# Performance work log

Hardware: AMD Instinct MI355X
Metric: run time of the kernel (lower is better)

## Reference

```python
import jax, jax.numpy as jnp
import numpy as np

B, F_C, F_F = 2, 32768, 131072
C_IN, C_OUT, W_DIM, COLOR = 128, 64, 512, 3
K2 = 9
PAD0, PAD1 = 192, 384
ACT_GAIN = float(np.sqrt(2.0))  # lrelu def_gain


def _gather(x, nbr, is_pad, pad):
    # x: [N, C]; nbr: [M, k] indices into [N + pad]; is_pad: [M, k] bool
    padded = jnp.concatenate([x, jnp.zeros((pad, x.shape[1]), x.dtype)], 0)
    g = padded[nbr]  # [M, k, C]
    return jnp.where(is_pad[..., None], jnp.zeros((), x.dtype), g)


def _affine(w, aw, ab):
    # StyleGAN FullyConnectedLayer: runtime weight gain 1/sqrt(fan_in), bias_init=1
    return w @ (aw.T * (1.0 / np.sqrt(aw.shape[1]))) + ab


def _modconv(xg, weight, styles, demodulate=True):
    # xg: [N, k, I]; weight: [O, I, 1, k]; styles: [B, I]
    n, k, ci = xg.shape
    w = weight[:, :, 0, :][None, :, :, :] * styles[:, None, :, None]  # [B,O,I,k]
    if demodulate:
        w = w * jax.lax.rsqrt(jnp.sum(w * w, axis=(2, 3), keepdims=True) + 1e-8)
    xb = xg.reshape(styles.shape[0], -1, k, ci)  # [B,F,k,I]
    return jnp.einsum('bfki,boik->bfo', xb, w).reshape(n, -1)


def _smooth_upsample(x, nbr, is_pad, pad, pool_map):
    # upsample coarse->fine via parent map, then masked neighborhood mean
    xf = x[pool_map]  # [N_fine, C]
    g = _gather(xf, nbr, is_pad, pad)  # [N_fine, k, C]
    cnt = jnp.maximum(jnp.sum(~is_pad, axis=1), 1).astype(x.dtype)
    return jnp.sum(g, axis=1) / cnt[:, None]


def _act(x, gain):
    # clamp_gain(lrelu(x), act_gain*gain, 256*gain)
    y = jnp.where(x >= 0, x, 0.2 * x)
    return jnp.clip(y * (ACT_GAIN * gain), -256.0 * gain, 256.0 * gain)


def setup_inputs():
    key = jax.random.key(0)
    ks = jax.random.split(key, 16)
    x = jax.random.normal(ks[0], (B * F_C, C_IN), jnp.float32)
    img = jax.random.normal(ks[1], (B * F_C, COLOR), jnp.float32)
    ws = jax.random.normal(ks[2], (B, 3, W_DIM), jnp.float32)
    fn0 = jax.random.randint(ks[3], (B * F_C, K2), 0, B * F_C + PAD0, jnp.int32)
    fn1 = jax.random.randint(ks[4], (B * F_F, K2), 0, B * F_F + PAD1, jnp.int32)
    fip0 = jax.random.bernoulli(ks[5], 0.05, (B * F_C, K2))
    fip1 = jax.random.bernoulli(ks[6], 0.05, (B * F_F, K2))
    pool_map0 = jax.random.randint(ks[7], (B * F_F,), 0, B * F_C, jnp.int32)
    a0_w = jax.random.normal(ks[8], (C_IN, W_DIM), jnp.float32)
    a0_b = jnp.ones((C_IN,), jnp.float32)
    W0 = jax.random.normal(ks[9], (C_OUT, C_IN, 1, K2), jnp.float32)
    b0 = jnp.zeros((C_OUT,), jnp.float32)
    ns0 = jnp.zeros((1,), jnp.float32)
    nc0 = jax.random.normal(ks[10], (F_F,), jnp.float32)
    a1_w = jax.random.normal(ks[11], (C_OUT, W_DIM), jnp.float32)
    a1_b = jnp.ones((C_OUT,), jnp.float32)
    W1 = jax.random.normal(ks[12], (C_OUT, C_OUT, 1, K2), jnp.float32)
    b1 = jnp.zeros((C_OUT,), jnp.float32)
    ns1 = jnp.zeros((1,), jnp.float32)
    nc1 = jax.random.normal(ks[13], (F_F,), jnp.float32)
    at_w = jax.random.normal(ks[14], (C_OUT, W_DIM), jnp.float32)
    at_b = jnp.ones((C_OUT,), jnp.float32)
    Wt = jax.random.normal(ks[15], (COLOR, C_OUT, 1, 1), jnp.float32)
    bt = jnp.zeros((COLOR,), jnp.float32)
    return {"x": x, "img": img, "ws": ws, "a0_w": a0_w, "a0_b": a0_b, "W0": W0,
            "b0": b0, "ns0": ns0, "nc0": nc0, "a1_w": a1_w, "a1_b": a1_b,
            "W1": W1, "b1": b1, "ns1": ns1, "nc1": nc1, "at_w": at_w,
            "at_b": at_b, "Wt": Wt, "bt": bt, "fn0": fn0, "fip0": fip0,
            "fn1": fn1, "fip1": fip1, "pool_map0": pool_map0,
            "pad0": PAD0, "pad1": PAD1}


def reference(x, img, ws, a0_w, a0_b, W0, b0, ns0, nc0, a1_w, a1_b, W1, b1, ns1,
              nc1, at_w, at_b, Wt, bt, fn0, fip0, fn1, fip1, pool_map0, pad0, pad1):
    b = ws.shape[0]
    w0, w1, w2 = ws[:, 0], ws[:, 1], ws[:, 2]
    # conv0: coarse gather -> mod conv -> smooth upsample to fine -> noise/bias/act
    s0 = _affine(w0, a0_w, a0_b)
    noise0 = jnp.tile(nc0[None, :], (b, 1)).reshape(-1, 1) * ns0  # noise_mode='const'
    h = _modconv(_gather(x, fn0, fip0, pad0), W0, s0)
    h = _smooth_upsample(h, fn1, fip1, pad1, pool_map0)
    h = _act(h + noise0 + b0[None, :], 1.0)
    # conv1: fine level, no resampler
    s1 = _affine(w1, a1_w, a1_b)
    noise1 = jnp.tile(nc1[None, :], (b, 1)).reshape(-1, 1) * ns1
    h = _modconv(_gather(h, fn1, fip1, pad1), W1, s1)
    h = _act(h + noise1 + b1[None, :], 1.0)
    # torgb: kernel_size=1 -> self index only, no demodulation
    st = _affine(w2, at_w, at_b) * (1.0 / np.sqrt(C_OUT))
    y = _modconv(_gather(h, fn1[:, :1], fip1[:, :1], pad1), Wt, st, demodulate=False)
    y = jnp.clip(y + bt[None, :], -256.0, 256.0)
    img = _smooth_upsample(img, fn1, fip1, pad1, pool_map0) + y
    return (h, img)
```

## Files before the change

### kernel.cpp

```cpp
#include <hip/hip_runtime.h>
#include <hip/hip_bf16.h>

constexpr int F_C   = 32768;
constexpr int F_F   = 131072;
constexpr int N0    = 65536;
constexpr int N1    = 262144;
constexpr int C_IN  = 128;
constexpr int W_DIM = 512;
constexpr int K2c   = 9;
constexpr float RS512     = 0.04419417382415922f;
constexpr float ACT_GAINc = 1.4142135623730951f;

constexpr size_t FO_S0  = 0;
constexpr size_t FO_S1  = 256;
constexpr size_t FO_ST  = 384;
constexpr size_t OFF_WM0T = 2048;
constexpr size_t OFF_WM1T = OFF_WM0T + 294912;
constexpr size_t OFF_H0   = 458752;
constexpr size_t OFF_HA   = OFF_H0 + (size_t)8388608;
constexpr size_t OFF_YPRE = OFF_H0;
constexpr size_t OFF_XB   = OFF_HA;

typedef short s16x8 __attribute__((ext_vector_type(8)));
typedef float f32x4 __attribute__((ext_vector_type(4)));

__device__ __forceinline__ float b2f(unsigned short u) {
    union { unsigned int i; float f; } v; v.i = ((unsigned int)u) << 16; return v.f;
}
__device__ __forceinline__ unsigned short f2b(float f) {
    __hip_bfloat16 h = __float2bfloat16(f);
    return *reinterpret_cast<unsigned short*>(&h);
}
__device__ __forceinline__ float waveRedSum(float v) {
    for (int m = 32; m; m >>= 1) v += __shfl_xor(v, m, 64);
    return v;
}
__device__ __forceinline__ float actf(float v) {
    float y = (v >= 0.f) ? v : 0.2f * v;
    y *= ACT_GAINc;
    return fminf(fmaxf(y, -256.f), 256.f);
}

__global__ __launch_bounds__(64)
void k_styles(const float* __restrict__ wsF,
              const float* __restrict__ a0w, const float* __restrict__ a0b,
              const float* __restrict__ a1w, const float* __restrict__ a1b,
              const float* __restrict__ atw, const float* __restrict__ atb,
              float* __restrict__ fr)
{
    int bid = blockIdx.x, lane = threadIdx.x;
    int bb, ii, ll, row; const float *aw, *ab; float* dst; float post = 1.f;
    if (bid < 256)      { bb = bid >> 7;             ii = bid & 127; ll = 0; aw = a0w; ab = a0b; dst = fr + FO_S0; row = 128; }
    else if (bid < 384) { int t = bid - 256; bb = t >> 6; ii = t & 63; ll = 1; aw = a1w; ab = a1b; dst = fr + FO_S1; row = 64; }
    else                { int t = bid - 384; bb = t >> 6; ii = t & 63; ll = 2; aw = atw; ab = atb; dst = fr + FO_ST; row = 64; post = 0.125f; }
    const float* wsv = wsF + (size_t)(bb * 3 + ll) * W_DIM;
    const float* awr = aw + (size_t)ii * W_DIM;
    float s = 0.f;
    for (int j = lane; j < W_DIM; j += 64) s += wsv[j] * awr[j];
    s = waveRedSum(s);
    if (lane == 0) dst[bb * row + ii] = (s * RS512 + ab[ii]) * post;
}

__global__ __launch_bounds__(256)
void k_wmod(const float* __restrict__ W0,
            const float* __restrict__ W1,
            const float* __restrict__ fr,
            unsigned short* __restrict__ wm0T,
            unsigned short* __restrict__ wm1T)
{
    int bo = blockIdx.x, tid = threadIdx.x;
    int b, o, CI, NE; const float* W; const float* S; unsigned short* dst;
    if (bo < 128) { b = bo >> 6; o = bo & 63; CI = 128; NE = 1152; W = W0; S = fr + FO_S0; dst = wm0T; }
    else { int t = bo - 128; b = t >> 6; o = t & 63; CI = 64; NE = 576; W = W1; S = fr + FO_S1; dst = wm1T; }
    const float* Wo = W + (size_t)o * NE;
    const float* Sb = S + (size_t)b * CI;
    float ss = 0.f;
    for (int idx = tid; idx < NE; idx += 256) {
        int i = idx / K2c;
        float p = Wo[idx] * Sb[i];
        ss += p * p;
    }
    __shared__ float red[4];
    float s = waveRedSum(ss);
    if ((tid & 63) == 0) red[tid >> 6] = s;
    __syncthreads();
    float d = rsqrtf(red[0] + red[1] + red[2] + red[3] + 1e-8f);
    for (int idx = tid; idx < NE; idx += 256) {
        int i = idx / K2c, kk = idx - i * K2c;
        dst[((size_t)(b * K2c + kk) * 64 + o) * CI + i] = f2b(Wo[idx] * Sb[i] * d);
    }
}

__global__ __launch_bounds__(256)
void k_xcvt(const float* __restrict__ xF, unsigned short* __restrict__ xB)
{
    int i = blockIdx.x * 256 + threadIdx.x;
    float4 f = ((const float4*)xF)[i];
    union { unsigned short u[4]; uint2 v; } t;
    t.u[0] = f2b(f.x); t.u[1] = f2b(f.y); t.u[2] = f2b(f.z); t.u[3] = f2b(f.w);
    ((uint2*)xB)[i] = t.v;
}

__global__ __launch_bounds__(256, 4)
void k_layer0(const unsigned short* __restrict__ xB,
              const int*  __restrict__ fn0,
              const int*  __restrict__ fip0,
              const unsigned short* __restrict__ wm0T,
              unsigned short* __restrict__ h0B)
{
    __shared__ unsigned short W_lds[9 * 64 * 64];
    const int tid  = threadIdx.x;
    const int g0   = blockIdx.x * 256;
    const int b    = g0 / F_C;
    const int wave = tid >> 6, lane = tid & 63;
    const int lg   = lane >> 4, lr = lane & 15;
    const int wbase = g0 + wave * 64;
    const unsigned short* wtap = wm0T + (size_t)b * K2c * 64 * C_IN;

    int nbrk[4][9];
    #pragma unroll
    for (int rg = 0; rg < 4; ++rg) {
        int row = wbase + rg * 16 + lr;
        #pragma unroll
        for (int k = 0; k < 9; ++k) {
            int fn = fn0[(size_t)row * 9 + k];
            int ip = fip0[(size_t)row * 9 + k];
            nbrk[rg][k] = (!ip && fn < N0) ? fn : -1;
        }
    }

    f32x4 acc[4][4] = {};
    for (int h = 0; h < 2; ++h) {
        __syncthreads();
        #pragma unroll
        for (int t = 0; t < 18; ++t) {
            int idx = tid + 256 * t;
            int tap = idx >> 9;
            int rem = idx & 511;
            int row = rem >> 3, cc = rem & 7;
            uint4 v = *(const uint4*)(wtap + ((size_t)tap * 64 + row) * C_IN + h * 64 + cc * 8);
            *(uint4*)(&W_lds[tap * 4096 + row * 64 + ((cc ^ (row & 7)) << 3)]) = v;
        }
        __syncthreads();
        #pragma unroll
        for (int kk = 0; kk < 9; ++kk) {
            s16x8 bf[2][4];
            #pragma unroll
            for (int c2 = 0; c2 < 2; ++c2)
                #pragma unroll
                for (int nt = 0; nt < 4; ++nt) {
                    int row = nt * 16 + lr;
                    bf[c2][nt] = *(const s16x8*)(&W_lds[kk * 4096 + row * 64 + (((c2 * 4 + lg) ^ (row & 7)) << 3)]);
                }
            #pragma unroll
            for (int rg = 0; rg < 4; ++rg) {
                int nbr = nbrk[rg][kk];
                int pc  = nbr >= 0 ? nbr : 0;
                const uint4* ap = (const uint4*)(xB + (size_t)pc * C_IN) + lg;
                uint4 a0 = ap[h * 8];
                uint4 a1 = ap[h * 8 + 4];
                if (nbr < 0) { a0 = uint4{0,0,0,0}; a1 = uint4{0,0,0,0}; }
                s16x8 af0 = *reinterpret_cast<const s16x8*>(&a0);
                s16x8 af1 = *reinterpret_cast<const s16x8*>(&a1);
                #pragma unroll
                for (int nt = 0; nt < 4; ++nt)
                    acc[rg][nt] = __builtin_amdgcn_mfma_f32_16x16x32_bf16(af0, bf[0][nt], acc[rg][nt], 0, 0, 0);
                #pragma unroll
                for (int nt = 0; nt < 4; ++nt)
                    acc[rg][nt] = __builtin_amdgcn_mfma_f32_16x16x32_bf16(af1, bf[1][nt], acc[rg][nt], 0, 0, 0);
            }
        }
    }
    #pragma unroll
    for (int rg = 0; rg < 4; ++rg)
        #pragma unroll
        for (int nt = 0; nt < 4; ++nt) {
            int o = nt * 16 + lr;
            #pragma unroll
            for (int r = 0; r < 4; ++r) {
                int node = wbase + rg * 16 + lg * 4 + r;
                h0B[(size_t)node * 64 + o] = f2b(acc[rg][nt][r]);
            }
        }
}

__global__ __launch_bounds__(256)
void k_ha(const unsigned short* __restrict__ h0B,
          const int*  __restrict__ fn1,
          const int*  __restrict__ fip1,
          const int*  __restrict__ pool,
          const float* __restrict__ nc0,
          const float* __restrict__ ns0,
          const float* __restrict__ b0,
          unsigned short* __restrict__ haB)
{
    __shared__ int   pmArr[288];
    __shared__ int   vArr[288];
    __shared__ float invCnt[32];
    const int tid = threadIdx.x;
    const int n0  = blockIdx.x * 32;
    for (int idx = tid; idx < 288; idx += 256) {
        int fn = fn1[(size_t)n0 * K2c + idx];
        int ip = fip1[(size_t)n0 * K2c + idx];
        int v  = !ip;
        int pm = -1;
        if (v && fn < N1) pm = pool[fn];
        pmArr[idx] = pm;
        vArr[idx]  = v;
    }
    __syncthreads();
    if (tid < 32) {
        int c = 0;
        #pragma unroll
        for (int k = 0; k < K2c; ++k) c += vArr[tid * K2c + k];
        invCnt[tid] = 1.f / (float)(c > 0 ? c : 1);
    }
    __syncthreads();
    const int wave = tid >> 6, lane = tid & 63;
    const float nsc  = ns0[0];
    const float bias = b0[lane];
    for (int jj = 0; jj < 8; ++jj) {
        int node = wave * 8 + jj;
        int g    = n0 + node;
        float acc = 0.f;
        #pragma unroll
        for (int k = 0; k < K2c; ++k) {
            int pm = pmArr[node * K2c + k];
            int pc = pm >= 0 ? pm : 0;
            float val = b2f(h0B[(size_t)pc * 64 + lane]);
            acc += (pm >= 0) ? val : 0.f;
        }
        float hu = acc * invCnt[node];
        float v  = hu + nc0[g & (F_F - 1)] * nsc + bias;
        haB[(size_t)g * 64 + lane] = f2b(actf(v));
    }
}

__global__ __launch_bounds__(512, 4)
void k_layer1(const unsigned short* __restrict__ haB,
              const int*  __restrict__ fn1,
              const int*  __restrict__ fip1,
              const unsigned short* __restrict__ wm1T,
              const float* __restrict__ nc1,
              const float* __restrict__ ns1,
              const float* __restrict__ b1,
              const float* __restrict__ stS,
              const float* __restrict__ WtF,
              float* __restrict__ hOut,
              float* __restrict__ yPre2)
{
    __shared__ unsigned short W_lds[9 * 64 * 64];
    const int tid  = threadIdx.x;
    const int g0   = blockIdx.x * 512;
    const int b    = g0 / F_F;
    const int wave = tid >> 6, lane = tid & 63;
    const int lg   = lane >> 4, lr = lane & 15;
    const int wbase = g0 + wave * 64;
    const unsigned short* wtap = wm1T + (size_t)b * K2c * 4096;

    #pragma unroll
    for (int t = 0; t < 9; ++t) {
        int idx = tid + 512 * t;
        int tap = idx >> 9;
        int rem = idx & 511;
        int row = rem >> 3, c = rem & 7;
        uint4 v = ((const uint4*)wtap)[idx];
        *(uint4*)(&W_lds[tap * 4096 + row * 64 + ((c ^ (row & 7)) << 3)]) = v;
    }

    int nbrk[4][9];
    #pragma unroll
    for (int rg = 0; rg < 4; ++rg) {
        int row = wbase + rg * 16 + lr;
        #pragma unroll
        for (int k = 0; k < 9; ++k) {
            int fn = fn1[(size_t)row * 9 + k];
            int ip = fip1[(size_t)row * 9 + k];
            nbrk[rg][k] = (!ip && fn < N1) ? fn : -1;
        }
    }
    __syncthreads();

    f32x4 acc[4][4] = {};
    #pragma unroll
    for (int kk = 0; kk < 9; ++kk) {
        s16x8 bf[2][4];
        #pragma unroll
        for (int h = 0; h < 2; ++h)
            #pragma unroll
            for (int nt = 0; nt < 4; ++nt) {
                int row = nt * 16 + lr;
                bf[h][nt] = *(const s16x8*)(&W_lds[kk * 4096 + row * 64 + (((h * 4 + lg) ^ (row & 7)) << 3)]);
            }
        #pragma unroll
        for (int rg = 0; rg < 4; ++rg) {
            int nbr = nbrk[rg][kk];
            int pc  = nbr >= 0 ? nbr : 0;
            const uint4* ap = (const uint4*)(haB + (size_t)pc * 64) + lg;
            uint4 a0 = ap[0], a1 = ap[4];
            if (nbr < 0) { a0 = uint4{0,0,0,0}; a1 = uint4{0,0,0,0}; }
            s16x8 af0 = *reinterpret_cast<const s16x8*>(&a0);
            s16x8 af1 = *reinterpret_cast<const s16x8*>(&a1);
            #pragma unroll
            for (int nt = 0; nt < 4; ++nt)
                acc[rg][nt] = __builtin_amdgcn_mfma_f32_16x16x32_bf16(af0, bf[0][nt], acc[rg][nt], 0, 0, 0);
            #pragma unroll
            for (int nt = 0; nt < 4; ++nt)
                acc[rg][nt] = __builtin_amdgcn_mfma_f32_16x16x32_bf16(af1, bf[1][nt], acc[rg][nt], 0, 0, 0);
        }
    }

    const float nsc = ns1[0];
    #pragma unroll
    for (int rg = 0; rg < 4; ++rg) {
        float p00[4] = {}, p01[4] = {}, p02[4] = {};
        float p10[4] = {}, p11[4] = {}, p12[4] = {};
        #pragma unroll
        for (int nt = 0; nt < 4; ++nt) {
            int o = nt * 16 + lr;
            float bias = b1[o];
            float st0  = stS[o], st1 = stS[64 + o];
            float wt0 = WtF[o], wt1 = WtF[64 + o], wt2 = WtF[128 + o];
            float w00 = wt0 * st0, w01 = wt1 * st0, w02 = wt2 * st0;
            float w10 = wt0 * st1, w11 = wt1 * st1, w12 = wt2 * st1;
            #pragma unroll
            for (int r = 0; r < 4; ++r) {
                int node = wbase + rg * 16 + lg * 4 + r;
                float v  = actf(acc[rg][nt][r] + nc1[node & (F_F - 1)] * nsc + bias);
                hOut[(size_t)node * 64 + o] = v;
                p00[r] += v * w00; p01[r] += v * w01; p02[r] += v * w02;
                p10[r] += v * w10; p11[r] += v * w11; p12[r] += v * w12;
            }
        }
        #pragma unroll
        for (int m = 1; m < 16; m <<= 1) {
            #pragma unroll
            for (int r = 0; r < 4; ++r) {
                p00[r] += __shfl_xor(p00[r], m, 64);
                p01[r] += __shfl_xor(p01[r], m, 64);
                p02[r] += __shfl_xor(p02[r], m, 64);
                p10[r] += __shfl_xor(p10[r], m, 64);
                p11[r] += __shfl_xor(p11[r], m, 64);
                p12[r] += __shfl_xor(p12[r], m, 64);
            }
        }
        if (lr == 0) {
            #pragma unroll
            for (int r = 0; r < 4; ++r) {
                int node = wbase + rg * 16 + lg * 4 + r;
                yPre2[(size_t)node * 6 + 0] = p00[r];
                yPre2[(size_t)node * 6 + 1] = p01[r];
                yPre2[(size_t)node * 6 + 2] = p02[r];
                yPre2[(size_t)node * 6 + 3] = p10[r];
                yPre2[(size_t)node * 6 + 4] = p11[r];
                yPre2[(size_t)node * 6 + 5] = p12[r];
            }
        }
    }
}

__global__ __launch_bounds__(256)
void k_rgb(const float* __restrict__ yPre2,
           const float* __restrict__ imgF,
           const int*  __restrict__ fn1,
           const int*  __restrict__ fip1,
           const int*  __restrict__ pool,
           const float* __restrict__ btF,
           float* __restrict__ outImg)
{
    const int n = blockIdx.x * 256 + threadIdx.x;
    const int bOut = n / F_F;
    int fn[K2c], ip[K2c];
    #pragma unroll
    for (int k = 0; k < K2c; ++k) {
        fn[k] = fn1[(size_t)n * K2c + k];
        ip[k] = fip1[(size_t)n * K2c + k];
    }
    int pm[K2c], cnt = 0;
    #pragma unroll
    for (int k = 0; k < K2c; ++k) {
        int v  = !ip[k];
        cnt   += v;
        pm[k]  = (v && fn[k] < N1) ? pool[fn[k]] : -1;
    }
    float sr = 0.f, sg = 0.f, sb = 0.f;
    #pragma unroll
    for (int k = 0; k < K2c; ++k) {
        int   pc = pm[k] >= 0 ? pm[k] : 0;
        float m  = pm[k] >= 0 ? 1.f : 0.f;
        sr += m * imgF[(size_t)pc * 3 + 0];
        sg += m * imgF[(size_t)pc * 3 + 1];
        sb += m * imgF[(size_t)pc * 3 + 2];
    }
    int nb0 = (!ip[0] && fn[0] < N1) ? fn[0] : -1;
    float y0 = 0.f, y1 = 0.f, y2 = 0.f;
    if (nb0 >= 0) {
        const float* yp = yPre2 + (size_t)nb0 * 6 + bOut * 3;
        y0 = yp[0]; y1 = yp[1]; y2 = yp[2];
    }
    float ic = 1.f / (float)(cnt > 0 ? cnt : 1);
    y0 = fminf(fmaxf(y0 + btF[0], -256.f), 256.f);
    y1 = fminf(fmaxf(y1 + btF[1], -256.f), 256.f);
    y2 = fminf(fmaxf(y2 + btF[2], -256.f), 256.f);
    outImg[(size_t)n * 3 + 0] = sr * ic + y0;
    outImg[(size_t)n * 3 + 1] = sg * ic + y1;
    outImg[(size_t)n * 3 + 2] = sb * ic + y2;
}

extern "C" void kernel_launch(void* const* d_in, const int* in_sizes, int n_in,
                              void* d_out, int out_size, void* d_ws, size_t ws_size,
                              hipStream_t stream)
{
    const float* xF   = (const float*)d_in[0];
    const float* imgF = (const float*)d_in[1];
    const float* wsF  = (const float*)d_in[2];
    const float* a0w  = (const float*)d_in[3];
    const float* a0b  = (const float*)d_in[4];
    const float* W0w  = (const float*)d_in[5];
    const float* b0w  = (const float*)d_in[6];
    const float* ns0  = (const float*)d_in[7];
    const float* nc0  = (const float*)d_in[8];
    const float* a1w  = (const float*)d_in[9];
    const float* a1b  = (const float*)d_in[10];
    const float* W1w  = (const float*)d_in[11];
    const float* b1w  = (const float*)d_in[12];
    const float* ns1  = (const float*)d_in[13];
    const float* nc1  = (const float*)d_in[14];
    const float* atw  = (const float*)d_in[15];
    const float* atb  = (const float*)d_in[16];
    const float* WtF  = (const float*)d_in[17];
    const float* btF  = (const float*)d_in[18];
    const int* fn0  = (const int*)d_in[19];
    const int* fip0 = (const int*)d_in[20];
    const int* fn1  = (const int*)d_in[21];
    const int* fip1 = (const int*)d_in[22];
    const int* pool = (const int*)d_in[23];

    char* wsb = (char*)d_ws;
    float* fr = (float*)wsb;
    unsigned short* wm0T = (unsigned short*)(wsb + OFF_WM0T);
    unsigned short* wm1T = (unsigned short*)(wsb + OFF_WM1T);
    unsigned short* h0B  = (unsigned short*)(wsb + OFF_H0);
    unsigned short* haB  = (unsigned short*)(wsb + OFF_HA);
    unsigned short* xB   = (unsigned short*)(wsb + OFF_XB);
    float* yPre2         = (float*)(wsb + OFF_YPRE);

    float* hOut   = (float*)d_out;
    float* imgOut = hOut + (size_t)N1 * 64;

    hipLaunchKernelGGL(k_styles, dim3(512), dim3(64), 0, stream,
                       wsF, a0w, a0b, a1w, a1b, atw, atb, fr);
    hipLaunchKernelGGL(k_wmod, dim3(256), dim3(256), 0, stream,
                       W0w, W1w, fr, wm0T, wm1T);
    hipLaunchKernelGGL(k_xcvt, dim3((N0 * C_IN) / 4 / 256), dim3(256), 0, stream,
                       xF, xB);
    hipLaunchKernelGGL(k_layer0, dim3(N0 / 256), dim3(256), 0, stream,
                       xB, fn0, fip0, wm0T, h0B);
    hipLaunchKernelGGL(k_ha, dim3(N1 / 32), dim3(256), 0, stream,
                       h0B, fn1, fip1, pool, nc0, ns0, b0w, haB);
    hipLaunchKernelGGL(k_layer1, dim3(N1 / 512), dim3(512), 0, stream,
                       haB, fn1, fip1, wm1T, nc1, ns1, b1w,
                       fr + FO_ST, WtF, hOut, yPre2);
    hipLaunchKernelGGL(k_rgb, dim3(N1 / 256), dim3(256), 0, stream,
                       yPre2, imgF, fn1, fip1, pool, btF, imgOut);
}
```

Before: 207.3 us.

## Split LDS weight staging into two tap phases to raise occupancy

Both conv kernels now stage the modulated weights into LDS in two phases (taps 0-4, then taps 5-8) instead of all nine taps at once. This cuts LDS per block from 72 KB to 40 KB so more blocks can be resident per CU. Layer1 also moves from 512-thread to 256-thread blocks. The cost is extra barriers and a second staging pass per half, during which the MFMA work stalls, and the staging loops are no longer fully unrolled.

```diff
diff --git a/kernel.cpp b/kernel.cpp
--- a/kernel.cpp
+++ b/kernel.cpp
@@ -108,7 +108,7 @@
               const unsigned short* __restrict__ wm0T,
               unsigned short* __restrict__ h0B)
 {
-    __shared__ unsigned short W_lds[9 * 64 * 64];
+    __shared__ unsigned short W_lds[5 * 4096];
     const int tid  = threadIdx.x;
     const int g0   = blockIdx.x * 256;
     const int b    = g0 / F_C;
@@ -130,47 +130,53 @@
     }
 
     f32x4 acc[4][4] = {};
+    auto stage = [&](int tapBase, int nTaps, int h) {
+        int nChunk = nTaps * 512;
+        for (int idx = tid; idx < nChunk; idx += 256) {
+            int tap = idx >> 9, rem = idx & 511;
+            int row = rem >> 3, cc = rem & 7;
+            uint4 v = *(const uint4*)(wtap + ((size_t)(tapBase + tap) * 64 + row) * C_IN + h * 64 + cc * 8);
+            *(uint4*)(&W_lds[tap * 4096 + row * 64 + ((cc ^ (row & 7)) << 3)]) = v;
+        }
+    };
+    auto computeTap = [&](int kk, int tapBase, int h) {
+        s16x8 bf[2][4];
+        #pragma unroll
+        for (int c2 = 0; c2 < 2; ++c2)
+            #pragma unroll
+            for (int nt = 0; nt < 4; ++nt) {
+                int row = nt * 16 + lr;
+                bf[c2][nt] = *(const s16x8*)(&W_lds[(kk - tapBase) * 4096 + row * 64 + (((c2 * 4 + lg) ^ (row & 7)) << 3)]);
+            }
+        #pragma unroll
+        for (int rg = 0; rg < 4; ++rg) {
+            int nbr = nbrk[rg][kk];
+            int pc  = nbr >= 0 ? nbr : 0;
+            const uint4* ap = (const uint4*)(xB + (size_t)pc * C_IN) + lg;
+            uint4 a0 = ap[h * 8], a1 = ap[h * 8 + 4];
+            if (nbr < 0) { a0 = uint4{0,0,0,0}; a1 = uint4{0,0,0,0}; }
+            s16x8 af0 = *reinterpret_cast<const s16x8*>(&a0);
+            s16x8 af1 = *reinterpret_cast<const s16x8*>(&a1);
+            #pragma unroll
+            for (int nt = 0; nt < 4; ++nt)
+                acc[rg][nt] = __builtin_amdgcn_mfma_f32_16x16x32_bf16(af0, bf[0][nt], acc[rg][nt], 0, 0, 0);
+            #pragma unroll
+            for (int nt = 0; nt < 4; ++nt)
+                acc[rg][nt] = __builtin_amdgcn_mfma_f32_16x16x32_bf16(af1, bf[1][nt], acc[rg][nt], 0, 0, 0);
+        }
+    };
+
     for (int h = 0; h < 2; ++h) {
         __syncthreads();
-        #pragma unroll
-        for (int t = 0; t < 18; ++t) {
-            int idx = tid + 256 * t;
-            int tap = idx >> 9;
-            int rem = idx & 511;
-            int row = rem >> 3, cc = rem & 7;
-            uint4 v = *(const uint4*)(wtap + ((size_t)tap * 64 + row) * C_IN + h * 64 + cc * 8);
-            *(uint4*)(&W_lds[tap * 4096 + row * 64 + ((cc ^ (row & 7)) << 3)]) = v;
-        }
+        stage(0, 5, h);
         __syncthreads();
-        #pragma unroll
-        for (int kk = 0; kk < 9; ++kk) {
-            s16x8 bf[2][4];
-            #pragma unroll
-            for (int c2 = 0; c2 < 2; ++c2)
-                #pragma unroll
-                for (int nt = 0; nt < 4; ++nt) {
-                    int row = nt * 16 + lr;
-                    bf[c2][nt] = *(const s16x8*)(&W_lds[kk * 4096 + row * 64 + (((c2 * 4 + lg) ^ (row & 7)) << 3)]);
-                }
-            #pragma unroll
-            for (int rg = 0; rg < 4; ++rg) {
-                int nbr = nbrk[rg][kk];
-                int pc  = nbr >= 0 ? nbr : 0;
-                const uint4* ap = (const uint4*)(xB + (size_t)pc * C_IN) + lg;
-                uint4 a0 = ap[h * 8];
-                uint4 a1 = ap[h * 8 + 4];
-                if (nbr < 0) { a0 = uint4{0,0,0,0}; a1 = uint4{0,0,0,0}; }
-                s16x8 af0 = *reinterpret_cast<const s16x8*>(&a0);
-                s16x8 af1 = *reinterpret_cast<const s16x8*>(&a1);
-                #pragma unroll
-                for (int nt = 0; nt < 4; ++nt)
-                    acc[rg][nt] = __builtin_amdgcn_mfma_f32_16x16x32_bf16(af0, bf[0][nt], acc[rg][nt], 0, 0, 0);
-                #pragma unroll
-                for (int nt = 0; nt < 4; ++nt)
-                    acc[rg][nt] = __builtin_amdgcn_mfma_f32_16x16x32_bf16(af1, bf[1][nt], acc[rg][nt], 0, 0, 0);
-            }
-        }
-    }
+        for (int kk = 0; kk < 5; ++kk) computeTap(kk, 0, h);
+        __syncthreads();
+        stage(5, 4, h);
+        __syncthreads();
+        for (int kk = 5; kk < 9; ++kk) computeTap(kk, 5, h);
+    }
+
     #pragma unroll
     for (int rg = 0; rg < 4; ++rg)
         #pragma unroll
@@ -236,7 +242,7 @@
     }
 }
 
-__global__ __launch_bounds__(512, 4)
+__global__ __launch_bounds__(256, 4)
 void k_layer1(const unsigned short* __restrict__ haB,
               const int*  __restrict__ fn1,
               const int*  __restrict__ fip1,
@@ -249,25 +255,15 @@
               float* __restrict__ hOut,
               float* __restrict__ yPre2)
 {
-    __shared__ unsigned short W_lds[9 * 64 * 64];
+    __shared__ unsigned short W_lds[5 * 4096];
     const int tid  = threadIdx.x;
-    const int g0   = blockIdx.x * 512;
+    const int g0   = blockIdx.x * 256;
     const int b    = g0 / F_F;
     const int wave = tid >> 6, lane = tid & 63;
     const int lg   = lane >> 4, lr = lane & 15;
     const int wbase = g0 + wave * 64;
     const unsigned short* wtap = wm1T + (size_t)b * K2c * 4096;
 
-    #pragma unroll
-    for (int t = 0; t < 9; ++t) {
-        int idx = tid + 512 * t;
-        int tap = idx >> 9;
-        int rem = idx & 511;
-        int row = rem >> 3, c = rem & 7;
-        uint4 v = ((const uint4*)wtap)[idx];
-        *(uint4*)(&W_lds[tap * 4096 + row * 64 + ((c ^ (row & 7)) << 3)]) = v;
-    }
-
     int nbrk[4][9];
     #pragma unroll
     for (int rg = 0; rg < 4; ++rg) {
@@ -279,18 +275,25 @@
             nbrk[rg][k] = (!ip && fn < N1) ? fn : -1;
         }
     }
-    __syncthreads();
 
     f32x4 acc[4][4] = {};
-    #pragma unroll
-    for (int kk = 0; kk < 9; ++kk) {
+    auto stage = [&](int tapBase, int nTaps) {
+        int nChunk = nTaps * 512;
+        for (int idx = tid; idx < nChunk; idx += 256) {
+            int tap = idx >> 9, rem = idx & 511;
+            int row = rem >> 3, c = rem & 7;
+            uint4 v = ((const uint4*)(wtap + (size_t)tapBase * 4096))[idx];
+            *(uint4*)(&W_lds[tap * 4096 + row * 64 + ((c ^ (row & 7)) << 3)]) = v;
+        }
+    };
+    auto computeTap = [&](int kk, int tapBase) {
         s16x8 bf[2][4];
         #pragma unroll
         for (int h = 0; h < 2; ++h)
             #pragma unroll
             for (int nt = 0; nt < 4; ++nt) {
                 int row = nt * 16 + lr;
-                bf[h][nt] = *(const s16x8*)(&W_lds[kk * 4096 + row * 64 + (((h * 4 + lg) ^ (row & 7)) << 3)]);
+                bf[h][nt] = *(const s16x8*)(&W_lds[(kk - tapBase) * 4096 + row * 64 + (((h * 4 + lg) ^ (row & 7)) << 3)]);
             }
         #pragma unroll
         for (int rg = 0; rg < 4; ++rg) {
@@ -308,7 +311,15 @@
             for (int nt = 0; nt < 4; ++nt)
                 acc[rg][nt] = __builtin_amdgcn_mfma_f32_16x16x32_bf16(af1, bf[1][nt], acc[rg][nt], 0, 0, 0);
         }
-    }
+    };
+
+    stage(0, 5);
+    __syncthreads();
+    for (int kk = 0; kk < 5; ++kk) computeTap(kk, 0);
+    __syncthreads();
+    stage(5, 4);
+    __syncthreads();
+    for (int kk = 5; kk < 9; ++kk) computeTap(kk, 5);
 
     const float nsc = ns1[0];
     #pragma unroll
@@ -458,7 +469,7 @@
                        xB, fn0, fip0, wm0T, h0B);
     hipLaunchKernelGGL(k_ha, dim3(N1 / 32), dim3(256), 0, stream,
                        h0B, fn1, fip1, pool, nc0, ns0, b0w, haB);
-    hipLaunchKernelGGL(k_layer1, dim3(N1 / 512), dim3(512), 0, stream,
+    hipLaunchKernelGGL(k_layer1, dim3(N1 / 256), dim3(256), 0, stream,
                        haB, fn1, fip1, wm1T, nc1, ns1, b1w,
                        fr + FO_ST, WtF, hOut, yPre2);
     hipLaunchKernelGGL(k_rgb, dim3(N1 / 256), dim3(256), 0, stream,
```

Result: slower. 316.1 us (+52.5%).

## Prefetch layer1 neighbor gathers two taps ahead and shrink blocks to 256

Applied to the files above, without the earlier changes.

k_layer1 now holds register double buffers of gathered neighbor rows and issues the loads for tap kk+2 before running the MFMAs for tap kk, so gather latency overlaps with matrix math. The block size drops from 512 to 256 threads, so twice as many blocks each load the full 9-tap weight set into LDS. Launch bounds for both layer kernels drop to 2 blocks per SM, freeing registers for the prefetch buffers. The cost is more redundant weight loads into LDS, possibly lower occupancy, and higher register pressure.

```diff
diff --git a/kernel.cpp b/kernel.cpp
--- a/kernel.cpp
+++ b/kernel.cpp
@@ -101,14 +101,14 @@
     ((uint2*)xB)[i] = t.v;
 }
 
-__global__ __launch_bounds__(256, 4)
+__global__ __launch_bounds__(256, 2)
 void k_layer0(const unsigned short* __restrict__ xB,
               const int*  __restrict__ fn0,
               const int*  __restrict__ fip0,
               const unsigned short* __restrict__ wm0T,
               unsigned short* __restrict__ h0B)
 {
-    __shared__ unsigned short W_lds[9 * 64 * 64];
+    __shared__ unsigned short W_lds[9 * 4096];
     const int tid  = threadIdx.x;
     const int g0   = blockIdx.x * 256;
     const int b    = g0 / F_C;
@@ -236,7 +236,7 @@
     }
 }
 
-__global__ __launch_bounds__(512, 4)
+__global__ __launch_bounds__(256, 2)
 void k_layer1(const unsigned short* __restrict__ haB,
               const int*  __restrict__ fn1,
               const int*  __restrict__ fip1,
@@ -249,9 +249,9 @@
               float* __restrict__ hOut,
               float* __restrict__ yPre2)
 {
-    __shared__ unsigned short W_lds[9 * 64 * 64];
+    __shared__ unsigned short W_lds[9 * 4096];
     const int tid  = threadIdx.x;
-    const int g0   = blockIdx.x * 512;
+    const int g0   = blockIdx.x * 256;
     const int b    = g0 / F_F;
     const int wave = tid >> 6, lane = tid & 63;
     const int lg   = lane >> 4, lr = lane & 15;
@@ -259,8 +259,8 @@
     const unsigned short* wtap = wm1T + (size_t)b * K2c * 4096;
 
     #pragma unroll
-    for (int t = 0; t < 9; ++t) {
-        int idx = tid + 512 * t;
+    for (int t = 0; t < 18; ++t) {
+        int idx = tid + 256 * t;
         int tap = idx >> 9;
         int rem = idx & 511;
         int row = rem >> 3, c = rem & 7;
@@ -279,25 +279,53 @@
             nbrk[rg][k] = (!ip && fn < N1) ? fn : -1;
         }
     }
-    __syncthreads();
-
-    f32x4 acc[4][4] = {};
-    #pragma unroll
-    for (int kk = 0; kk < 9; ++kk) {
-        s16x8 bf[2][4];
-        #pragma unroll
-        for (int h = 0; h < 2; ++h)
-            #pragma unroll
-            for (int nt = 0; nt < 4; ++nt) {
-                int row = nt * 16 + lr;
-                bf[h][nt] = *(const s16x8*)(&W_lds[kk * 4096 + row * 64 + (((h * 4 + lg) ^ (row & 7)) << 3)]);
-            }
+
+    uint4 pa[2][4][2];
+    #pragma unroll
+    for (int kk = 0; kk < 2; ++kk)
         #pragma unroll
         for (int rg = 0; rg < 4; ++rg) {
             int nbr = nbrk[rg][kk];
             int pc  = nbr >= 0 ? nbr : 0;
             const uint4* ap = (const uint4*)(haB + (size_t)pc * 64) + lg;
-            uint4 a0 = ap[0], a1 = ap[4];
+            pa[kk][rg][0] = ap[0];
+            pa[kk][rg][1] = ap[4];
+        }
+
+    __syncthreads();
+
+    f32x4 acc[4][4] = {};
+    #pragma unroll
+    for (int kk = 0; kk < 9; ++kk) {
+        const int slot = kk & 1;
+        s16x8 bf[2][4];
+        #pragma unroll
+        for (int h = 0; h < 2; ++h)
+            #pragma unroll
+            for (int nt = 0; nt < 4; ++nt) {
+                int row = nt * 16 + lr;
+                bf[h][nt] = *(const s16x8*)(&W_lds[kk * 4096 + row * 64 + (((h * 4 + lg) ^ (row & 7)) << 3)]);
+            }
+        uint4 cur[4][2];
+        #pragma unroll
+        for (int rg = 0; rg < 4; ++rg) {
+            cur[rg][0] = pa[slot][rg][0];
+            cur[rg][1] = pa[slot][rg][1];
+        }
+        if (kk + 2 < 9) {
+            #pragma unroll
+            for (int rg = 0; rg < 4; ++rg) {
+                int nbr = nbrk[rg][kk + 2];
+                int pc  = nbr >= 0 ? nbr : 0;
+                const uint4* ap = (const uint4*)(haB + (size_t)pc * 64) + lg;
+                pa[slot][rg][0] = ap[0];
+                pa[slot][rg][1] = ap[4];
+            }
+        }
+        #pragma unroll
+        for (int rg = 0; rg < 4; ++rg) {
+            int nbr = nbrk[rg][kk];
+            uint4 a0 = cur[rg][0], a1 = cur[rg][1];
             if (nbr < 0) { a0 = uint4{0,0,0,0}; a1 = uint4{0,0,0,0}; }
             s16x8 af0 = *reinterpret_cast<const s16x8*>(&a0);
             s16x8 af1 = *reinterpret_cast<const s16x8*>(&a1);
@@ -458,7 +486,7 @@
                        xB, fn0, fip0, wm0T, h0B);
     hipLaunchKernelGGL(k_ha, dim3(N1 / 32), dim3(256), 0, stream,
                        h0B, fn1, fip1, pool, nc0, ns0, b0w, haB);
-    hipLaunchKernelGGL(k_layer1, dim3(N1 / 512), dim3(512), 0, stream,
+    hipLaunchKernelGGL(k_layer1, dim3(N1 / 256), dim3(256), 0, stream,
                        haB, fn1, fip1, wm1T, nc1, ns1, b1w,
                        fr + FO_ST, WtF, hOut, yPre2);
     hipLaunchKernelGGL(k_rgb, dim3(N1 / 256), dim3(256), 0, stream,
```

Result: faster. 191.9 us (-7.4%).
